# Kernel tuning notes

Measured on AMD Instinct MI355X. Metric: run time of the kernel, lower is better.

Reference implementation:

```python
import jax, jax.numpy as jnp
import numpy as np

EPS = 1e-8          # torch CosineSimilarity eps
TEMPERATURE = 0.5
N = 4096            # device_size (== batch_size, world_size=1)
D = 256             # projection embedding dim


def setup_inputs() -> dict:
    key = jax.random.key(0)
    k1, k2 = jax.random.split(key)
    return {
        "z_i": jax.random.normal(k1, (N, D), dtype=jnp.float32),
        "z_j": jax.random.normal(k2, (N, D), dtype=jnp.float32),
    }


def reference(z_i, z_j):
    n = z_i.shape[0]
    # z_large = [z_i ; z_j]  (world_size == 1 layout)
    z = jnp.concatenate([z_i, z_j], axis=0)                      # [2N, D]
    zn = z / jnp.maximum(jnp.linalg.norm(z, axis=1, keepdims=True), EPS)
    zi_n, zj_n = zn[:n], zn[n:]
    # cosine similarity via normalize + GEMM (same math as CosineSimilarity(dim=2))
    sim_i = (zi_n @ zn.T) / TEMPERATURE                          # [N, 2N]
    sim_j = (zj_n @ zn.T) / TEMPERATURE                          # [N, 2N]
    idx = jnp.arange(n)
    neg_inf = jnp.finfo(sim_i.dtype).min
    # positives: sim_i row i vs column N+i; sim_j row i vs column i
    pos_i = sim_i[idx, n + idx]                                  # [N]
    pos_j = sim_j[idx, idx]                                      # [N]
    # exclude self-similarity from the softmax denominator
    sim_i_m = sim_i.at[idx, idx].set(neg_inf)
    sim_j_m = sim_j.at[idx, n + idx].set(neg_inf)
    # CrossEntropyLoss(sum) with label 0 on [pos, negs] == sum(lse - pos)
    lse_i = jax.scipy.special.logsumexp(sim_i_m, axis=1)
    lse_j = jax.scipy.special.logsumexp(sim_j_m, axis=1)
    loss_i = jnp.sum(lse_i - pos_i) / n
    loss_j = jnp.sum(lse_j - pos_j) / n
    return loss_i, loss_j
```

## Files before the change

### kernel.cpp

```cpp
#include <hip/hip_runtime.h>

#define NN   4096
#define TWON 8192
#define DD   256
#define TINV 2.0f
#define SCALE 1.69864363f
#define CS   16

typedef __attribute__((ext_vector_type(8)))  short v8s;
typedef __attribute__((ext_vector_type(16))) float v16f;

__device__ inline unsigned short f2bf(float f) {
  unsigned int u = __float_as_uint(f);
  u += 0x7FFFu + ((u >> 16) & 1u);
  return (unsigned short)(u >> 16);
}

__global__ void k_normpos(const float* __restrict__ zi, const float* __restrict__ zj,
                          unsigned short* __restrict__ zn, float* __restrict__ pospart) {
  int wid = threadIdx.x >> 6, lane = threadIdx.x & 63;
  int pr  = blockIdx.x * 2 + (wid >> 1);
  int isj = wid & 1;
  const float* src = (isj ? zj : zi) + (size_t)pr * DD;
  float4 v = *(const float4*)(src + lane * 4);
  float ss = v.x*v.x + v.y*v.y + v.z*v.z + v.w*v.w;
  #pragma unroll
  for (int m = 1; m < 64; m <<= 1) ss += __shfl_xor(ss, m, 64);
  float nrm = fmaxf(sqrtf(ss), 1e-8f);

  __shared__ float zbuf[2][DD];
  __shared__ float nbuf[2];
  if (!isj) {
    *(float4*)&zbuf[wid >> 1][lane * 4] = v;
    if (lane == 0) nbuf[wid >> 1] = nrm;
  }

  float sc = SCALE / nrm;
  ushort4 o;
  o.x = f2bf(v.x * sc); o.y = f2bf(v.y * sc);
  o.z = f2bf(v.z * sc); o.w = f2bf(v.w * sc);
  int zrow = (isj ? NN : 0) + pr;
  *(ushort4*)(zn + (size_t)zrow * DD + lane * 4) = o;

  __syncthreads();
  if (isj) {
    float4 a = *(const float4*)&zbuf[wid >> 1][lane * 4];
    float d = a.x*v.x + a.y*v.y + a.z*v.z + a.w*v.w;
    #pragma unroll
    for (int m = 1; m < 64; m <<= 1) d += __shfl_xor(d, m, 64);
    if (lane == 0) pospart[pr] = d * TINV / (nbuf[wid >> 1] * nrm);
  }
}

__global__ __launch_bounds__(256, 2) void k_main(const unsigned short* __restrict__ zn,
                                                 float* __restrict__ wsum) {
  const char* znb = (const char*)zn;
  int tid = threadIdx.x, wid = tid >> 6, lane = tid & 63;
  int rb = blockIdx.x >> 4, cs = blockIdx.x & 15;
  int wrow0 = rb * 256 + wid * 64;
  int lr = lane & 31, lg = lane >> 5;
  int cbase = cs * 512;
  int lane_src = lr * 512 + lg * 16;

  v8s afrag[2][16];
  #pragma unroll
  for (int h = 0; h < 2; ++h) {
    #pragma unroll
    for (int kk = 0; kk < 16; ++kk) {
      size_t off = (size_t)(wrow0 + h * 32 + lr) * 512 + kk * 32 + lg * 16;
      afrag[h][kk] = *(const v8s*)(znb + off);
    }
  }

  __shared__ char tiles[4][16384];
  v16f sumv0, sumv1;
  #pragma unroll
  for (int q = 0; q < 16; ++q) { sumv0[q] = 0.f; sumv1[q] = 0.f; }

#define STAGE(CT, BI) { \
    size_t gb = (size_t)(cbase + (CT) * 32) * 512; \
    _Pragma("unroll") \
    for (int p = 0; p < 4; ++p) { \
      int ti = wid * 4 + p; \
      const char* sp = znb + gb + ti * 32 + lane_src; \
      __builtin_amdgcn_global_load_lds((const __attribute__((address_space(1))) void*)sp, \
          (__attribute__((address_space(3))) void*)&tiles[BI][ti * 1024], 16, 0, 0); \
    } }

  STAGE(0, 0);
  STAGE(1, 1);
  STAGE(2, 2);

  #pragma unroll 1
  for (int t = 0; t < 16; ++t) {
    if (t <= 13)      asm volatile("s_waitcnt vmcnt(8)" ::: "memory");
    else if (t == 14) asm volatile("s_waitcnt vmcnt(4)" ::: "memory");
    else              asm volatile("s_waitcnt vmcnt(0)" ::: "memory");
    __builtin_amdgcn_sched_barrier(0);
    __builtin_amdgcn_s_barrier();
    __builtin_amdgcn_sched_barrier(0);

    if (t + 3 < 16) { STAGE(t + 3, ((t + 3) & 3)); }

    int bi = t & 3;
    int ctile = cbase + t * 32;
    v16f acc0, acc1;
    #pragma unroll
    for (int q = 0; q < 16; ++q) { acc0[q] = 0.f; acc1[q] = 0.f; }
    const char* bb = &tiles[bi][lg * 512 + lr * 16];
    __builtin_amdgcn_s_setprio(1);
    #pragma unroll
    for (int kk = 0; kk < 16; ++kk) {
      v8s b = *(const v8s*)(bb + kk * 1024);
      acc0 = __builtin_amdgcn_mfma_f32_32x32x16_bf16(afrag[0][kk], b, acc0, 0, 0, 0);
      acc1 = __builtin_amdgcn_mfma_f32_32x32x16_bf16(afrag[1][kk], b, acc1, 0, 0, 0);
    }
    __builtin_amdgcn_s_setprio(0);

    if (ctile == wrow0 || ctile == wrow0 + 32) {
      bool h0 = (ctile == wrow0);
      #pragma unroll
      for (int q = 0; q < 16; ++q) {
        int ro = 4 * lg + (q & 3) + 8 * (q >> 2);
        float e0 = __builtin_amdgcn_exp2f(acc0[q]);
        float e1 = __builtin_amdgcn_exp2f(acc1[q]);
        if (h0 && ro == lr) e0 = 0.f;
        if (!h0 && ro == lr) e1 = 0.f;
        sumv0[q] += e0; sumv1[q] += e1;
      }
    } else {
      #pragma unroll
      for (int q = 0; q < 16; ++q) {
        sumv0[q] += __builtin_amdgcn_exp2f(acc0[q]);
        sumv1[q] += __builtin_amdgcn_exp2f(acc1[q]);
      }
    }
  }
#undef STAGE

  #pragma unroll
  for (int q = 0; q < 16; ++q) {
    float v0 = sumv0[q], v1 = sumv1[q];
    #pragma unroll
    for (int m = 1; m < 32; m <<= 1) {
      v0 += __shfl_xor(v0, m, 64);
      v1 += __shfl_xor(v1, m, 64);
    }
    sumv0[q] = v0; sumv1[q] = v1;
  }
  if (lr < 16) {
    int qi = lr;
    float o0 = 0.f, o1 = 0.f;
    #pragma unroll
    for (int q = 0; q < 16; ++q) {
      o0 = (q == qi) ? sumv0[q] : o0;
      o1 = (q == qi) ? sumv1[q] : o1;
    }
    int ro = 4 * lg + (qi & 3) + 8 * (qi >> 2);
    wsum[(size_t)(wrow0 + ro) * CS + cs] = o0;
    wsum[(size_t)(wrow0 + 32 + ro) * CS + cs] = o1;
  }
}

__global__ void k_lse(const float* __restrict__ wsum, float* __restrict__ lsepart) {
  int tid = threadIdx.x;
  int row = blockIdx.x * 128 + tid;
  const float4* p = (const float4*)(wsum + (size_t)row * CS);
  float4 a = p[0], b = p[1], c = p[2], d = p[3];
  float s = (((a.x + a.y) + (a.z + a.w)) + ((b.x + b.y) + (b.z + b.w)))
          + (((c.x + c.y) + (c.z + c.w)) + ((d.x + d.y) + (d.z + d.w)));
  float lse = logf(s);
  #pragma unroll
  for (int m = 1; m < 64; m <<= 1) lse += __shfl_xor(lse, m, 64);
  __shared__ float sb[2];
  if ((tid & 63) == 0) sb[tid >> 6] = lse;
  __syncthreads();
  if (tid == 0) lsepart[blockIdx.x] = sb[0] + sb[1];
}

__global__ void k_final(const float* __restrict__ lsepart, const float* __restrict__ pospart,
                        float* __restrict__ out) {
  int tid = threadIdx.x, wid = tid >> 6, lane = tid & 63;
  float li = (tid < 32) ? lsepart[tid] : 0.f;
  float lj = (tid >= 32 && tid < 64) ? lsepart[tid] : 0.f;
  float pp = 0.f;
  #pragma unroll
  for (int k = 0; k < 16; ++k) pp += pospart[tid + 256 * k];
  #pragma unroll
  for (int m = 1; m < 64; m <<= 1) {
    li += __shfl_xor(li, m, 64);
    lj += __shfl_xor(lj, m, 64);
    pp += __shfl_xor(pp, m, 64);
  }
  __shared__ float sI[4], sJ[4], sP[4];
  if (lane == 0) { sI[wid] = li; sJ[wid] = lj; sP[wid] = pp; }
  __syncthreads();
  if (tid == 0) {
    float SI = (sI[0] + sI[1]) + (sI[2] + sI[3]);
    float SJ = (sJ[0] + sJ[1]) + (sJ[2] + sJ[3]);
    float SP = (sP[0] + sP[1]) + (sP[2] + sP[3]);
    out[0] = (SI - SP) * (1.0f / NN);
    out[1] = (SJ - SP) * (1.0f / NN);
  }
}

extern "C" void kernel_launch(void* const* d_in, const int* in_sizes, int n_in,
                              void* d_out, int out_size, void* d_ws, size_t ws_size,
                              hipStream_t stream) {
  const float* zi = (const float*)d_in[0];
  const float* zj = (const float*)d_in[1];
  float* out = (float*)d_out;
  char* ws = (char*)d_ws;
  unsigned short* zn = (unsigned short*)ws;
  float* pospart = (float*)(ws + 4194304);
  float* lsepart = (float*)(ws + 4210688);
  float* wsum    = (float*)(ws + 4210944);

  k_normpos<<<2048, 256, 0, stream>>>(zi, zj, zn, pospart);
  k_main<<<512, 256, 0, stream>>>(zn, wsum);
  k_lse<<<64, 128, 0, stream>>>(wsum, lsepart);
  k_final<<<1, 256, 0, stream>>>(lsepart, pospart, out);
}
```

Before: 54.95 us.

## Halve per-wave row tile to 32 and split K across two accumulators

Each wave now covers 32 rows instead of 64, and the grid doubles to 1024 blocks. The K loop splits into even and odd accumulators that are summed before the exp, which shortens the dependent MFMA chain. This cuts register use and raises parallelism. In exchange, each B tile loaded into LDS is reused by half as many rows, so total LDS and global traffic for B doubles.

After: 61.62 us. +12.1%, slower.

```diff
diff --git a/kernel.cpp b/kernel.cpp
--- a/kernel.cpp
+++ b/kernel.cpp
@@ -57,25 +57,22 @@
   const char* znb = (const char*)zn;
   int tid = threadIdx.x, wid = tid >> 6, lane = tid & 63;
   int rb = blockIdx.x >> 4, cs = blockIdx.x & 15;
-  int wrow0 = rb * 256 + wid * 64;
+  int wrow0 = rb * 128 + wid * 32;
   int lr = lane & 31, lg = lane >> 5;
   int cbase = cs * 512;
   int lane_src = lr * 512 + lg * 16;
 
-  v8s afrag[2][16];
-  #pragma unroll
-  for (int h = 0; h < 2; ++h) {
-    #pragma unroll
-    for (int kk = 0; kk < 16; ++kk) {
-      size_t off = (size_t)(wrow0 + h * 32 + lr) * 512 + kk * 32 + lg * 16;
-      afrag[h][kk] = *(const v8s*)(znb + off);
-    }
+  v8s afrag[16];
+  #pragma unroll
+  for (int kk = 0; kk < 16; ++kk) {
+    size_t off = (size_t)(wrow0 + lr) * 512 + kk * 32 + lg * 16;
+    afrag[kk] = *(const v8s*)(znb + off);
   }
 
   __shared__ char tiles[4][16384];
-  v16f sumv0, sumv1;
-  #pragma unroll
-  for (int q = 0; q < 16; ++q) { sumv0[q] = 0.f; sumv1[q] = 0.f; }
+  v16f sumv;
+  #pragma unroll
+  for (int q = 0; q < 16; ++q) sumv[q] = 0.f;
 
 #define STAGE(CT, BI) { \
     size_t gb = (size_t)(cbase + (CT) * 32) * 512; \
@@ -104,61 +101,50 @@
 
     int bi = t & 3;
     int ctile = cbase + t * 32;
-    v16f acc0, acc1;
-    #pragma unroll
-    for (int q = 0; q < 16; ++q) { acc0[q] = 0.f; acc1[q] = 0.f; }
+    v16f acce, acco;
+    #pragma unroll
+    for (int q = 0; q < 16; ++q) { acce[q] = 0.f; acco[q] = 0.f; }
     const char* bb = &tiles[bi][lg * 512 + lr * 16];
     __builtin_amdgcn_s_setprio(1);
     #pragma unroll
-    for (int kk = 0; kk < 16; ++kk) {
-      v8s b = *(const v8s*)(bb + kk * 1024);
-      acc0 = __builtin_amdgcn_mfma_f32_32x32x16_bf16(afrag[0][kk], b, acc0, 0, 0, 0);
-      acc1 = __builtin_amdgcn_mfma_f32_32x32x16_bf16(afrag[1][kk], b, acc1, 0, 0, 0);
+    for (int kk = 0; kk < 16; kk += 2) {
+      v8s be = *(const v8s*)(bb + kk * 1024);
+      v8s bo = *(const v8s*)(bb + (kk + 1) * 1024);
+      acce = __builtin_amdgcn_mfma_f32_32x32x16_bf16(afrag[kk],     be, acce, 0, 0, 0);
+      acco = __builtin_amdgcn_mfma_f32_32x32x16_bf16(afrag[kk + 1], bo, acco, 0, 0, 0);
     }
     __builtin_amdgcn_s_setprio(0);
 
-    if (ctile == wrow0 || ctile == wrow0 + 32) {
-      bool h0 = (ctile == wrow0);
+    if (ctile == wrow0) {
       #pragma unroll
       for (int q = 0; q < 16; ++q) {
         int ro = 4 * lg + (q & 3) + 8 * (q >> 2);
-        float e0 = __builtin_amdgcn_exp2f(acc0[q]);
-        float e1 = __builtin_amdgcn_exp2f(acc1[q]);
-        if (h0 && ro == lr) e0 = 0.f;
-        if (!h0 && ro == lr) e1 = 0.f;
-        sumv0[q] += e0; sumv1[q] += e1;
+        float e = __builtin_amdgcn_exp2f(acce[q] + acco[q]);
+        if (ro == lr) e = 0.f;
+        sumv[q] += e;
       }
     } else {
       #pragma unroll
-      for (int q = 0; q < 16; ++q) {
-        sumv0[q] += __builtin_amdgcn_exp2f(acc0[q]);
-        sumv1[q] += __builtin_amdgcn_exp2f(acc1[q]);
-      }
+      for (int q = 0; q < 16; ++q)
+        sumv[q] += __builtin_amdgcn_exp2f(acce[q] + acco[q]);
     }
   }
 #undef STAGE
 
   #pragma unroll
   for (int q = 0; q < 16; ++q) {
-    float v0 = sumv0[q], v1 = sumv1[q];
-    #pragma unroll
-    for (int m = 1; m < 32; m <<= 1) {
-      v0 += __shfl_xor(v0, m, 64);
-      v1 += __shfl_xor(v1, m, 64);
-    }
-    sumv0[q] = v0; sumv1[q] = v1;
+    float v0 = sumv[q];
+    #pragma unroll
+    for (int m = 1; m < 32; m <<= 1) v0 += __shfl_xor(v0, m, 64);
+    sumv[q] = v0;
   }
   if (lr < 16) {
     int qi = lr;
-    float o0 = 0.f, o1 = 0.f;
-    #pragma unroll
-    for (int q = 0; q < 16; ++q) {
-      o0 = (q == qi) ? sumv0[q] : o0;
-      o1 = (q == qi) ? sumv1[q] : o1;
-    }
+    float o0 = 0.f;
+    #pragma unroll
+    for (int q = 0; q < 16; ++q) o0 = (q == qi) ? sumv[q] : o0;
     int ro = 4 * lg + (qi & 3) + 8 * (qi >> 2);
     wsum[(size_t)(wrow0 + ro) * CS + cs] = o0;
-    wsum[(size_t)(wrow0 + 32 + ro) * CS + cs] = o1;
   }
 }
 
@@ -217,7 +203,7 @@
   float* wsum    = (float*)(ws + 4210944);
 
   k_normpos<<<2048, 256, 0, stream>>>(zi, zj, zn, pospart);
-  k_main<<<512, 256, 0, stream>>>(zn, wsum);
+  k_main<<<1024, 256, 0, stream>>>(zn, wsum);
   k_lse<<<64, 128, 0, stream>>>(wsum, lsepart);
   k_final<<<1, 256, 0, stream>>>(lsepart, pospart, out);
 }
```
